# Optimization experiments

Hardware: AMD Instinct MI355X
Metric: run time of the kernel (lower is better)

Reference implementation:

```python
import jax, jax.numpy as jnp
import numpy as np

DIM, N_HEADS, N_KV, HEAD_DIM = 4096, 32, 8, 128
REPEATS = N_HEADS // N_KV
SCALE = HEAD_DIM ** -0.5


def apply_rope(x, offset=0):
    # x: [b, h, l, hd]; rotation convention matches the torch source:
    # out_even = xe*cos + xo*sin, out_odd = -xe*sin + xo*cos, interleaved back.
    hd = x.shape[-1]
    l = x.shape[2]
    freqs = 1.0 / 10000.0 ** (jnp.arange(0, hd, 2, dtype=jnp.float32) / hd)  # [hd/2]
    t = jnp.arange(l, dtype=jnp.float32) + offset
    ang = t[:, None] * freqs[None, :]                     # [l, hd/2]
    sin, cos = jnp.sin(ang), jnp.cos(ang)
    xe, xo = x[..., 0::2], x[..., 1::2]                   # [b,h,l,hd/2]
    out = jnp.stack([xe * cos + xo * sin, -xe * sin + xo * cos], axis=-1)
    return out.reshape(x.shape)


def setup_inputs() -> dict:
    key = jax.random.key(0)
    ks = jax.random.split(key, 5)
    b, l = 1, 2048
    x = jax.random.normal(ks[0], (b, l, DIM), dtype=jnp.float32)
    # additive causal mask: 0 on/below diagonal, -1e9 above
    neg = jnp.full((l, l), -1e9, dtype=jnp.float32)
    mask = jnp.triu(neg, k=1)
    wq = jax.random.normal(ks[1], (N_HEADS * HEAD_DIM, DIM), dtype=jnp.float32) * 0.02
    wk = jax.random.normal(ks[2], (N_KV * HEAD_DIM, DIM), dtype=jnp.float32) * 0.02
    wv = jax.random.normal(ks[3], (N_KV * HEAD_DIM, DIM), dtype=jnp.float32) * 0.02
    wo = jax.random.normal(ks[4], (DIM, N_HEADS * HEAD_DIM), dtype=jnp.float32) * 0.02
    return {"x": x, "mask": mask, "wq": wq, "wk": wk, "wv": wv, "wo": wo}


def reference(x, mask, wq, wk, wv, wo):
    b, l, d = x.shape
    q = (x @ wq.T).reshape(b, l, N_HEADS, HEAD_DIM).transpose(0, 2, 1, 3)  # [b,H,l,hd]
    k = (x @ wk.T).reshape(b, l, N_KV, HEAD_DIM).transpose(0, 2, 1, 3)     # [b,Hk,l,hd]
    v = (x @ wv.T).reshape(b, l, N_KV, HEAD_DIM).transpose(0, 2, 1, 3)
    # GQA repeat (head = kv_head*repeats + r, same as torch cat+view)
    k = jnp.repeat(k, REPEATS, axis=1)
    v = jnp.repeat(v, REPEATS, axis=1)
    q = apply_rope(q)
    k = apply_rope(k)
    atn = jnp.einsum('bhqd,bhkd->bhqk', q * SCALE, k) + mask
    atn = jax.nn.softmax(atn.astype(jnp.float32), axis=-1).astype(q.dtype)
    out = jnp.einsum('bhqk,bhkd->bhqd', atn, v)
    out = out.transpose(0, 2, 1, 3).reshape(b, l, -1)
    return (out @ wo.T, k, v)
```

## Files before the change

### kernel.cpp

```cpp
#include <hip/hip_runtime.h>
#include <stdint.h>

#define L_SEQ  2048
#define NHEAD  32
#define NKV    8
#define HD     128
#define DIM    4096
#define KVDIM  1024
#define QKVS   6144
#define SCALE  0.08838834764831845f
#define LOG2E  1.4426950408889634f
#define SM_OFF 12.0f

typedef __attribute__((ext_vector_type(8))) short bf16x8;
typedef __attribute__((ext_vector_type(4))) float f32x4;

#define FENCE() asm volatile("" ::: "memory")

__device__ __forceinline__ unsigned short f2bf(float f) {
    unsigned u = __float_as_uint(f);
    u = (u + 0x7FFFu + ((u >> 16) & 1u)) >> 16;
    return (unsigned short)u;
}
__device__ __forceinline__ float bf2f(unsigned short h) {
    return __uint_as_float(((unsigned)h) << 16);
}
__device__ __forceinline__ void gload_lds16(const void* g, void* l) {
    __builtin_amdgcn_global_load_lds(
        (const __attribute__((address_space(1))) unsigned int*)g,
        (__attribute__((address_space(3))) unsigned int*)l, 16, 0, 0);
}

__global__ void cvt_all(const float* __restrict__ x,  const float* __restrict__ wq,
                        const float* __restrict__ wk, const float* __restrict__ wv,
                        unsigned short* __restrict__ xb, unsigned short* __restrict__ wqb,
                        unsigned short* __restrict__ wkvb) {
    const int N_X = L_SEQ * DIM / 4, N_WQ = DIM * DIM / 4, N_WKV = KVDIM * DIM / 4;
    int i = blockIdx.x * blockDim.x + threadIdx.x;
    int stride = gridDim.x * blockDim.x;
    const int total = N_X + N_WQ + 2 * N_WKV;
    for (; i < total; i += stride) {
        const float* src; unsigned short* dst; int j = i;
        if (j < N_X)                { src = x;  dst = xb; }
        else if ((j -= N_X) < N_WQ) { src = wq; dst = wqb; }
        else if ((j -= N_WQ) < N_WKV) { src = wk; dst = wkvb; }
        else { j -= N_WKV; src = wv; dst = wkvb + (size_t)KVDIM * DIM; }
        float4 v = ((const float4*)src)[j];
        ushort4 o;
        o.x = f2bf(v.x); o.y = f2bf(v.y); o.z = f2bf(v.z); o.w = f2bf(v.w);
        ((ushort4*)dst)[j] = o;
    }
}

__global__ void cvt_f32_bf16(const float* __restrict__ in, unsigned short* __restrict__ out, int n4) {
    int i = blockIdx.x * blockDim.x + threadIdx.x;
    int stride = gridDim.x * blockDim.x;
    for (; i < n4; i += stride) {
        float4 v = ((const float4*)in)[i];
        ushort4 o;
        o.x = f2bf(v.x); o.y = f2bf(v.y); o.z = f2bf(v.z); o.w = f2bf(v.w);
        ((ushort4*)out)[i] = o;
    }
}

__global__ void addf32(float* __restrict__ out, const float* __restrict__ p, int n4) {
    int i = blockIdx.x * blockDim.x + threadIdx.x;
    int stride = gridDim.x * blockDim.x;
    for (; i < n4; i += stride) {
        float4 a = ((const float4*)out)[i];
        float4 b = ((const float4*)p)[i];
        a.x += b.x; a.y += b.y; a.z += b.z; a.w += b.w;
        ((float4*)out)[i] = a;
    }
}

__global__ void rope_table(float2* __restrict__ rt) {
    int i = blockIdx.x * blockDim.x + threadIdx.x;
    if (i >= L_SEQ * 64) return;
    int l = i >> 6, f = i & 63;
    float freq = powf(10000.0f, -(float)f / 64.0f);
    float ang  = (float)l * freq;
    rt[i] = make_float2(cosf(ang), sinf(ang));
}

__global__ void rope_all(unsigned short* __restrict__ QKVp, const float2* __restrict__ rt,
                         float* __restrict__ KO) {
    const int qNum = L_SEQ * NHEAD * 64;
    int i = blockIdx.x * blockDim.x + threadIdx.x;
    if (i < qNum) {
        int f  = i & 63;
        int hh = (i >> 6) & 31;
        int l  = i >> 11;
        float2 cs = rt[(l << 6) + f];
        size_t base = (size_t)l * QKVS + (hh << 7);
        float xe = bf2f(QKVp[base + 2 * f]);
        float xo = bf2f(QKVp[base + 2 * f + 1]);
        const float mul = SCALE * LOG2E;
        QKVp[base + 2 * f]     = f2bf((xe * cs.x + xo * cs.y) * mul);
        QKVp[base + 2 * f + 1] = f2bf((-xe * cs.y + xo * cs.x) * mul);
    } else {
        int j  = i - qNum;
        int f  = j & 63;
        int hh = (j >> 6) & 7;
        int l  = j >> 9;
        float2 cs = rt[(l << 6) + f];
        size_t base = (size_t)l * QKVS + 4096 + (hh << 7);
        float xe = bf2f(QKVp[base + 2 * f]);
        float xo = bf2f(QKVp[base + 2 * f + 1]);
        unsigned short k0 = f2bf(xe * cs.x + xo * cs.y);
        unsigned short k1 = f2bf(-xe * cs.y + xo * cs.x);
        QKVp[base + 2 * f]     = k0;
        QKVp[base + 2 * f + 1] = k1;
        float k0f = bf2f(k0), k1f = bf2f(k1);
#pragma unroll
        for (int r = 0; r < 4; ++r) {
            size_t ko = ((size_t)(hh * 4 + r) * L_SEQ + l) * HD + 2 * f;
            KO[ko]     = k0f;
            KO[ko + 1] = k1f;
        }
    }
}

__global__ void vtrans(const unsigned short* __restrict__ KVp, unsigned short* __restrict__ VT,
                       float* __restrict__ VO) {
    __shared__ unsigned short t[32][33];
    int lt = blockIdx.x * 32;
    int h8 = blockIdx.y >> 2;
    int dt = (blockIdx.y & 3) * 32;
    int tx = threadIdx.x & 31, ty = threadIdx.x >> 5;
#pragma unroll
    for (int yy = ty; yy < 32; yy += 8) {
        unsigned short v = KVp[(size_t)(lt + yy) * QKVS + KVDIM + h8 * HD + dt + tx];
        t[yy][tx] = v;
        float vf = bf2f(v);
#pragma unroll
        for (int r = 0; r < 4; ++r)
            VO[((size_t)(h8 * 4 + r) * L_SEQ + lt + yy) * HD + dt + tx] = vf;
    }
    __syncthreads();
#pragma unroll
    for (int yy = ty; yy < 32; yy += 8)
        VT[(size_t)(h8 * HD + dt + yy) * L_SEQ + lt + tx] = t[tx][yy];
}

template <typename OT, int NF, int MG, int NG>
__global__ __launch_bounds__(512, 2) void gemm_8ph(const unsigned short* __restrict__ A,
                                                   const unsigned short* __restrict__ B,
                                                   OT* __restrict__ C0, OT* __restrict__ C1,
                                                   int N, int K, int klen) {
    __shared__ __align__(16) char L[65536 + 2 * NF * 8192];
    const int tid = threadIdx.x;
    const int w = tid >> 6, lane = tid & 63;
    const int gx = gridDim.x;
    const int orig = blockIdx.y * gx + blockIdx.x;
    const int xcd = orig & 7, j = orig >> 3;
    const int sm = gridDim.y / MG, sn = gx / NG;
    const int m0 = ((xcd / NG) * sm + j / sn) * 256;
    const int n0 = ((xcd % NG) * sn + j % sn) * (NF * 64);
    const int kbase = blockIdx.z * klen;
    OT* __restrict__ C = blockIdx.z ? C1 : C0;
    const int wr = (w >> 2) & 1;
    const int wc = w & 3;
    const int lr = lane & 15, lg = lane >> 4;
    const int NKT = klen >> 6;
    const int swb = (lr & 7) << 4;

    auto stageA = [&](int slot, int u, int kt) {
        int r  = u * 64 + w * 8 + (lane >> 3);
        int cg = (lane & 7) ^ (r & 7);
        gload_lds16(A + (size_t)(m0 + r) * K + kbase + kt * 64 + cg * 8,
                    L + slot * 32768 + (u * 64 + w * 8) * 128);
    };
    auto stageB = [&](int slot, int u, int kt) {
        int r  = u * 64 + w * 8 + (lane >> 3);
        int cg = (lane & 7) ^ (r & 7);
        gload_lds16(B + (size_t)(n0 + r) * K + kbase + kt * 64 + cg * 8,
                    L + 65536 + slot * (NF * 8192) + (u * 64 + w * 8) * 128);
    };

    const f32x4 fz = {0.f, 0.f, 0.f, 0.f};
    f32x4 acc[8][NF];
#pragma unroll
    for (int m = 0; m < 8; ++m)
#pragma unroll
        for (int n = 0; n < NF; ++n) acc[m][n] = fz;

    bf16x8 bfr[NF][2];

#pragma unroll
    for (int u = 0; u < 4; ++u) stageA(0, u, 0);
#pragma unroll
    for (int u = 0; u < NF; ++u) stageB(0, u, 0);
    if (NKT > 1) {
#pragma unroll
        for (int u = 0; u < NF; ++u) stageB(1, u, 1);
    }
    if constexpr (NF == 4) asm volatile("s_waitcnt vmcnt(4)" ::: "memory");
    else                   asm volatile("s_waitcnt vmcnt(3)" ::: "memory");

    for (int kt0 = 0; kt0 < NKT; kt0 += 2) {
#pragma unroll
        for (int kp = 0; kp < 2; ++kp) {
            const int kt = kt0 + kp;
            const int s = kp;
            const char* Abase = L + s * 32768;
            const char* Bbase = L + 65536 + s * (NF * 8192);
#pragma unroll
            for (int q = 0; q < 4; ++q) {
                FENCE();
                __builtin_amdgcn_s_barrier();
                FENCE();
                if (q == 0 && kt + 1 < NKT) { stageA(s ^ 1, 0, kt + 1); stageA(s ^ 1, 1, kt + 1); }
                if (q == 1 && kt + 1 < NKT) { stageA(s ^ 1, 2, kt + 1); stageA(s ^ 1, 3, kt + 1); }
                if (q == 2 && kt + 2 < NKT) { stageB(s, 0, kt + 2); stageB(s, 1, kt + 2); }
                if (q == 3 && kt + 2 < NKT) {
                    stageB(s, 2, kt + 2);
                    if constexpr (NF == 4) stageB(s, 3, kt + 2);
                }
                bf16x8 af[2][2];
#pragma unroll
                for (int mm = 0; mm < 2; ++mm)
#pragma unroll
                    for (int kk = 0; kk < 2; ++kk) {
                        int r = wr * 128 + (q * 2 + mm) * 16 + lr;
                        int b = (kk * 64 + lg * 16) ^ swb;
                        af[mm][kk] = *(const bf16x8*)(Abase + r * 128 + b);
                    }
                if (q == 0) {
#pragma unroll
                    for (int n = 0; n < NF; ++n)
#pragma unroll
                        for (int kk = 0; kk < 2; ++kk) {
                            int r = wc * (NF * 16) + n * 16 + lr;
                            int b = (kk * 64 + lg * 16) ^ swb;
                            bfr[n][kk] = *(const bf16x8*)(Bbase + r * 128 + b);
                        }
                }
                if (q == 3) {
                    if (kt + 2 < NKT) {
                        if constexpr (NF == 4) asm volatile("s_waitcnt vmcnt(4)" ::: "memory");
                        else                   asm volatile("s_waitcnt vmcnt(3)" ::: "memory");
                    } else {
                        asm volatile("s_waitcnt vmcnt(0)" ::: "memory");
                    }
                }
                __builtin_amdgcn_s_setprio(1);
#pragma unroll
                for (int mm = 0; mm < 2; ++mm)
#pragma unroll
                    for (int n = 0; n < NF; ++n)
#pragma unroll
                        for (int kk = 0; kk < 2; ++kk)
                            acc[q * 2 + mm][n] = __builtin_amdgcn_mfma_f32_16x16x32_bf16(
                                af[mm][kk], bfr[n][kk], acc[q * 2 + mm][n], 0, 0, 0);
                __builtin_amdgcn_s_setprio(0);
            }
        }
    }
#pragma unroll
    for (int m = 0; m < 8; ++m) {
        int mrow = m0 + wr * 128 + m * 16 + lg * 4;
#pragma unroll
        for (int n = 0; n < NF; ++n) {
            int ncol = n0 + wc * (NF * 16) + n * 16 + lr;
#pragma unroll
            for (int r = 0; r < 4; ++r) {
                float v = acc[m][n][r];
                if constexpr (sizeof(OT) == 2) C[(size_t)(mrow + r) * N + ncol] = f2bf(v);
                else                           C[(size_t)(mrow + r) * N + ncol] = v;
            }
        }
    }
}

__global__ __launch_bounds__(256, 4) void attn_fwd(const unsigned short* __restrict__ Q,
                                                   const unsigned short* __restrict__ KVp,
                                                   const unsigned short* __restrict__ VT,
                                                   unsigned short* __restrict__ AO) {
    __shared__ __align__(16) unsigned short Ks[64 * 128];
    __shared__ __align__(16) unsigned short Vs[128 * 64];
    __shared__ __align__(16) unsigned short P[4][16][64];
    const int tid = threadIdx.x, w = tid >> 6, lane = tid & 63;
    const int idx = blockIdx.x;
    const int h8  = idx & 7;
    const int h   = (h8 << 2) + ((idx >> 3) & 3);
    const int u   = idx >> 5;
    const int t   = u & 7, quart = u >> 3;
    const int qb  = (quart == 0) ? 31 - t : (quart == 1) ? 16 + t
                  : (quart == 2) ? 15 - t : t;
    const int lr = lane & 15, lg = lane >> 4;
    const int r0 = qb * 64 + w * 16;

    bf16x8 qf[4];
    {
        const unsigned short* qrow = Q + (size_t)(r0 + lr) * QKVS + h * HD + lg * 8;
#pragma unroll
        for (int kd = 0; kd < 4; ++kd) qf[kd] = *(const bf16x8*)(qrow + kd * 32);
    }

    bf16x8 ones;
#pragma unroll
    for (int z = 0; z < 8; ++z) ones[z] = (short)0x3F80;

    const f32x4 fz = {0.f, 0.f, 0.f, 0.f};
    f32x4 o[9];
#pragma unroll
    for (int nd = 0; nd < 9; ++nd) o[nd] = fz;

    const int nkv = qb + 1;
    for (int kv = 0; kv < nkv; ++kv) {
        const int kv0 = kv * 64;
#pragma unroll
        for (int c = 0; c < 4; ++c) {
            int krow = w * 16 + c * 4 + (lane >> 4);
            int kcg  = (lane & 15) ^ (krow & 7);
            gload_lds16(KVp + (size_t)(kv0 + krow) * QKVS + h8 * HD + kcg * 8,
                        Ks + (w * 16 + c * 4) * 128);
            int vrow = w * 32 + c * 8 + (lane >> 3);
            int vcg  = (lane & 7) ^ (vrow & 7);
            gload_lds16(VT + (size_t)(h8 * HD + vrow) * L_SEQ + kv0 + vcg * 8,
                        Vs + (w * 32 + c * 8) * 64);
        }
        __syncthreads();
        f32x4 s[4];
#pragma unroll
        for (int ni = 0; ni < 4; ++ni) s[ni] = fz;
        __builtin_amdgcn_s_setprio(1);
#pragma unroll
        for (int ni = 0; ni < 4; ++ni) {
            bf16x8 kf[4];
#pragma unroll
            for (int kd = 0; kd < 4; ++kd)
                kf[kd] = *(const bf16x8*)(Ks + (ni * 16 + lr) * 128 +
                                          (((kd * 4 + lg) ^ (lr & 7)) * 8));
#pragma unroll
            for (int kd = 0; kd < 4; ++kd)
                s[ni] = __builtin_amdgcn_mfma_f32_16x16x32_bf16(qf[kd], kf[kd], s[ni], 0, 0, 0);
        }
        __builtin_amdgcn_s_setprio(0);
        {
            const bool need_mask = (kv0 + 63) > r0;
#pragma unroll
            for (int ni = 0; ni < 4; ++ni)
#pragma unroll
                for (int rr = 0; rr < 4; ++rr) {
                    float p = __builtin_amdgcn_exp2f(s[ni][rr] - SM_OFF);
                    if (need_mask) {
                        int col = kv0 + ni * 16 + lr;
                        int row = r0 + lg * 4 + rr;
                        p = (col > row) ? 0.f : p;
                    }
                    s[ni][rr] = p;
                }
            char* Pb = (char*)&P[w][0][0];
#pragma unroll
            for (int ni = 0; ni < 4; ni += 2)
#pragma unroll
                for (int rr = 0; rr < 4; ++rr) {
                    unsigned pk;
                    asm("v_cvt_pk_bf16_f32 %0, %1, %2" : "=v"(pk) : "v"(s[ni][rr]), "v"(s[ni + 1][rr]));
                    const int row = lg * 4 + rr;
                    const int sw = (row & 7) << 4;
                    *(unsigned short*)(Pb + ((row * 128 + (ni * 16 + lr) * 2) ^ sw)) = (unsigned short)pk;
                    *(unsigned short*)(Pb + ((row * 128 + ((ni + 1) * 16 + lr) * 2) ^ sw)) =
                        (unsigned short)(pk >> 16);
                }
        }
        bf16x8 pa[2];
        {
            const char* Pb = (const char*)&P[w][0][0];
            const int swr = (lr & 7) << 4;
#pragma unroll
            for (int ks = 0; ks < 2; ++ks)
                pa[ks] = *(const bf16x8*)(Pb + ((lr * 128 + ks * 64 + lg * 16) ^ swr));
        }
        __builtin_amdgcn_s_setprio(1);
#pragma unroll
        for (int nd = 0; nd < 8; ++nd) {
            bf16x8 vf[2];
#pragma unroll
            for (int ks = 0; ks < 2; ++ks)
                vf[ks] = *(const bf16x8*)(Vs + (nd * 16 + lr) * 64 +
                                          (((ks * 4 + lg) ^ (lr & 7)) * 8));
#pragma unroll
            for (int ks = 0; ks < 2; ++ks)
                o[nd] = __builtin_amdgcn_mfma_f32_16x16x32_bf16(pa[ks], vf[ks], o[nd], 0, 0, 0);
        }
#pragma unroll
        for (int ks = 0; ks < 2; ++ks)
            o[8] = __builtin_amdgcn_mfma_f32_16x16x32_bf16(pa[ks], ones, o[8], 0, 0, 0);
        __builtin_amdgcn_s_setprio(0);
        __syncthreads();
    }
    {
        float inv[4];
#pragma unroll
        for (int rr = 0; rr < 4; ++rr) inv[rr] = 1.0f / o[8][rr];
#pragma unroll
        for (int nd = 0; nd < 8; ++nd)
#pragma unroll
            for (int rr = 0; rr < 4; ++rr) {
                int row = r0 + lg * 4 + rr;
                AO[(size_t)row * DIM + h * HD + nd * 16 + lr] = f2bf(o[nd][rr] * inv[rr]);
            }
    }
}

extern "C" void kernel_launch(void* const* d_in, const int* in_sizes, int n_in,
                              void* d_out, int out_size, void* d_ws, size_t ws_size,
                              hipStream_t stream) {
    (void)in_sizes; (void)n_in; (void)out_size; (void)ws_size;
    const float* x  = (const float*)d_in[0];
    const float* wq = (const float*)d_in[2];
    const float* wk = (const float*)d_in[3];
    const float* wv = (const float*)d_in[4];
    const float* wo = (const float*)d_in[5];

    float* out = (float*)d_out;
    float* KO  = out + (size_t)L_SEQ * DIM;
    float* VO  = KO + (size_t)NHEAD * L_SEQ * HD;

    char* ws = (char*)d_ws;
    const size_t MB = 1024 * 1024;
    unsigned short* xb   = (unsigned short*)(ws);
    unsigned short* wqb  = (unsigned short*)(ws + 16 * MB);
    unsigned short* wkvb = (unsigned short*)(ws + 48 * MB);
    unsigned short* qkvp = (unsigned short*)(ws + 64 * MB);
    unsigned short* vtb  = (unsigned short*)(ws + 88 * MB);
    float2*         rt   = (float2*)(ws + 92 * MB);
    unsigned short* aob  = xb;
    unsigned short* wob  = wqb;
    unsigned short* kvp  = qkvp + KVDIM * 4;
    float*          pko  = (float*)(ws + 48 * MB);

    cvt_all<<<2048, 256, 0, stream>>>(x, wq, wk, wv, xb, wqb, wkvb);
    rope_table<<<(L_SEQ * 64) / 256, 256, 0, stream>>>(rt);

    gemm_8ph<unsigned short, 3, 2, 4><<<dim3(QKVS / 192, L_SEQ / 256, 1), 512, 0, stream>>>(
        xb, wqb, qkvp, qkvp, QKVS, DIM, DIM);
    cvt_f32_bf16<<<2048, 256, 0, stream>>>(wo, wob, DIM * DIM / 4);

    rope_all<<<(L_SEQ * (NHEAD + NKV) * 64) / 256, 256, 0, stream>>>(qkvp, rt, KO);

    vtrans<<<dim3(L_SEQ / 32, 32), 256, 0, stream>>>(kvp, vtb, VO);

    attn_fwd<<<1024, 256, 0, stream>>>(qkvp, kvp, vtb, aob);

    gemm_8ph<float, 4, 2, 4><<<dim3(DIM / 256, L_SEQ / 256, 2), 512, 0, stream>>>(
        aob, wob, out, pko, DIM, DIM, DIM / 2);
    addf32<<<2048, 256, 0, stream>>>(out, pko, L_SEQ * DIM / 4);
}
```

Measured before the change: 312.6 us.

## Halve GEMM barrier phases and replace split-K reduction with atomic adds

The GEMM inner loop goes from four barrier-separated phases per k-tile to two. Each phase now loads four A fragments and issues twice as many MFMAs, and A and B staging is grouped into fewer, larger batches. The split-K output GEMM now atomically adds both halves into a zeroed output buffer, which removes the separate partial buffer and the addf32 pass. The cost is a memset, atomic traffic on the fp32 output, more register pressure from the larger fragment arrays, and a nondeterministic summation order.

```diff
diff --git a/kernel.cpp b/kernel.cpp
--- a/kernel.cpp
+++ b/kernel.cpp
@@ -60,17 +60,6 @@
         ushort4 o;
         o.x = f2bf(v.x); o.y = f2bf(v.y); o.z = f2bf(v.z); o.w = f2bf(v.w);
         ((ushort4*)out)[i] = o;
-    }
-}
-
-__global__ void addf32(float* __restrict__ out, const float* __restrict__ p, int n4) {
-    int i = blockIdx.x * blockDim.x + threadIdx.x;
-    int stride = gridDim.x * blockDim.x;
-    for (; i < n4; i += stride) {
-        float4 a = ((const float4*)out)[i];
-        float4 b = ((const float4*)p)[i];
-        a.x += b.x; a.y += b.y; a.z += b.z; a.w += b.w;
-        ((float4*)out)[i] = a;
     }
 }
 
@@ -143,8 +132,8 @@
         VT[(size_t)(h8 * HD + dt + yy) * L_SEQ + lt + tx] = t[tx][yy];
 }
 
-template <typename OT, int NF, int MG, int NG>
-__global__ __launch_bounds__(512, 2) void gemm_8ph(const unsigned short* __restrict__ A,
+template <typename OT, int NF, int MG, int NG, bool ATOMIC>
+__global__ __launch_bounds__(512, 2) void gemm_2ph(const unsigned short* __restrict__ A,
                                                    const unsigned short* __restrict__ B,
                                                    OT* __restrict__ C0, OT* __restrict__ C1,
                                                    int N, int K, int klen) {
@@ -158,7 +147,7 @@
     const int m0 = ((xcd / NG) * sm + j / sn) * 256;
     const int n0 = ((xcd % NG) * sn + j % sn) * (NF * 64);
     const int kbase = blockIdx.z * klen;
-    OT* __restrict__ C = blockIdx.z ? C1 : C0;
+    OT* __restrict__ C = (ATOMIC || blockIdx.z == 0) ? C0 : C1;
     const int wr = (w >> 2) & 1;
     const int wc = w & 3;
     const int lr = lane & 15, lg = lane >> 4;
@@ -206,23 +195,24 @@
             const char* Abase = L + s * 32768;
             const char* Bbase = L + 65536 + s * (NF * 8192);
 #pragma unroll
-            for (int q = 0; q < 4; ++q) {
+            for (int q = 0; q < 2; ++q) {
                 FENCE();
                 __builtin_amdgcn_s_barrier();
                 FENCE();
-                if (q == 0 && kt + 1 < NKT) { stageA(s ^ 1, 0, kt + 1); stageA(s ^ 1, 1, kt + 1); }
-                if (q == 1 && kt + 1 < NKT) { stageA(s ^ 1, 2, kt + 1); stageA(s ^ 1, 3, kt + 1); }
-                if (q == 2 && kt + 2 < NKT) { stageB(s, 0, kt + 2); stageB(s, 1, kt + 2); }
-                if (q == 3 && kt + 2 < NKT) {
-                    stageB(s, 2, kt + 2);
-                    if constexpr (NF == 4) stageB(s, 3, kt + 2);
-                }
-                bf16x8 af[2][2];
-#pragma unroll
-                for (int mm = 0; mm < 2; ++mm)
+                if (q == 0 && kt + 1 < NKT) {
+#pragma unroll
+                    for (int u = 0; u < 4; ++u) stageA(s ^ 1, u, kt + 1);
+                }
+                if (q == 1 && kt + 2 < NKT) {
+#pragma unroll
+                    for (int u = 0; u < NF; ++u) stageB(s, u, kt + 2);
+                }
+                bf16x8 af[4][2];
+#pragma unroll
+                for (int mm = 0; mm < 4; ++mm)
 #pragma unroll
                     for (int kk = 0; kk < 2; ++kk) {
-                        int r = wr * 128 + (q * 2 + mm) * 16 + lr;
+                        int r = wr * 128 + (q * 4 + mm) * 16 + lr;
                         int b = (kk * 64 + lg * 16) ^ swb;
                         af[mm][kk] = *(const bf16x8*)(Abase + r * 128 + b);
                     }
@@ -236,7 +226,7 @@
                             bfr[n][kk] = *(const bf16x8*)(Bbase + r * 128 + b);
                         }
                 }
-                if (q == 3) {
+                if (q == 1) {
                     if (kt + 2 < NKT) {
                         if constexpr (NF == 4) asm volatile("s_waitcnt vmcnt(4)" ::: "memory");
                         else                   asm volatile("s_waitcnt vmcnt(3)" ::: "memory");
@@ -246,13 +236,13 @@
                 }
                 __builtin_amdgcn_s_setprio(1);
 #pragma unroll
-                for (int mm = 0; mm < 2; ++mm)
+                for (int mm = 0; mm < 4; ++mm)
 #pragma unroll
                     for (int n = 0; n < NF; ++n)
 #pragma unroll
                         for (int kk = 0; kk < 2; ++kk)
-                            acc[q * 2 + mm][n] = __builtin_amdgcn_mfma_f32_16x16x32_bf16(
-                                af[mm][kk], bfr[n][kk], acc[q * 2 + mm][n], 0, 0, 0);
+                            acc[q * 4 + mm][n] = __builtin_amdgcn_mfma_f32_16x16x32_bf16(
+                                af[mm][kk], bfr[n][kk], acc[q * 4 + mm][n], 0, 0, 0);
                 __builtin_amdgcn_s_setprio(0);
             }
         }
@@ -266,8 +256,13 @@
 #pragma unroll
             for (int r = 0; r < 4; ++r) {
                 float v = acc[m][n][r];
-                if constexpr (sizeof(OT) == 2) C[(size_t)(mrow + r) * N + ncol] = f2bf(v);
-                else                           C[(size_t)(mrow + r) * N + ncol] = v;
+                if constexpr (sizeof(OT) == 2) {
+                    C[(size_t)(mrow + r) * N + ncol] = f2bf(v);
+                } else if constexpr (ATOMIC) {
+                    unsafeAtomicAdd((float*)&C[(size_t)(mrow + r) * N + ncol], v);
+                } else {
+                    C[(size_t)(mrow + r) * N + ncol] = v;
+                }
             }
         }
     }
@@ -431,12 +426,12 @@
     unsigned short* aob  = xb;
     unsigned short* wob  = wqb;
     unsigned short* kvp  = qkvp + KVDIM * 4;
-    float*          pko  = (float*)(ws + 48 * MB);
 
     cvt_all<<<2048, 256, 0, stream>>>(x, wq, wk, wv, xb, wqb, wkvb);
+    hipMemsetAsync(out, 0, (size_t)L_SEQ * DIM * sizeof(float), stream);
     rope_table<<<(L_SEQ * 64) / 256, 256, 0, stream>>>(rt);
 
-    gemm_8ph<unsigned short, 3, 2, 4><<<dim3(QKVS / 192, L_SEQ / 256, 1), 512, 0, stream>>>(
+    gemm_2ph<unsigned short, 3, 2, 4, false><<<dim3(QKVS / 192, L_SEQ / 256, 1), 512, 0, stream>>>(
         xb, wqb, qkvp, qkvp, QKVS, DIM, DIM);
     cvt_f32_bf16<<<2048, 256, 0, stream>>>(wo, wob, DIM * DIM / 4);
 
@@ -446,7 +441,6 @@
 
     attn_fwd<<<1024, 256, 0, stream>>>(qkvp, kvp, vtb, aob);
 
-    gemm_8ph<float, 4, 2, 4><<<dim3(DIM / 256, L_SEQ / 256, 2), 512, 0, stream>>>(
-        aob, wob, out, pko, DIM, DIM, DIM / 2);
-    addf32<<<2048, 256, 0, stream>>>(out, pko, L_SEQ * DIM / 4);
-}
+    gemm_2ph<float, 4, 2, 4, true><<<dim3(DIM / 256, L_SEQ / 256, 2), 512, 0, stream>>>(
+        aob, wob, out, out, DIM, DIM, DIM / 2);
+}
```

New measurement: 347.7 us. 1.11x slower.
